# Kernel optimization log

Measured on AMD Instinct MI355X. Metric: run time of the kernel, lower is better.

Reference implementation:

```python
import jax, jax.numpy as jnp
import numpy as np
import math

B, T, IN_DIM = 2, 2048, 512
D, NH, MULT, N_LAYER = 512, 8, 4, 3
N = D * MULT // NH  # per-head latent dim = 256
OUT_DIM = 512
THETA = 2 ** 16


def get_freqs(n):
    t = jnp.arange(n, dtype=jnp.float32)
    q = jnp.floor(t / 2.0) * 2.0  # quantize(q=2)
    return 1.0 / (THETA ** (q / n)) / (2.0 * math.pi)


def ln(x, eps=1e-5):
    mu = jnp.mean(x, axis=-1, keepdims=True)
    var = jnp.var(x, axis=-1, keepdims=True)
    return (x - mu) * jax.lax.rsqrt(var + eps)


def rope(phases, v):
    # phases: [T, N] broadcastable to v [B, nh, T, N]
    p = (phases % 1.0) * (2.0 * math.pi)
    pc, ps = jnp.cos(p), jnp.sin(p)
    # interleave rotate: out[..., 2i] = -v[..., 2i+1], out[..., 2i+1] = v[..., 2i]
    v_rot = jnp.stack((-v[..., 1::2], v[..., ::2]), axis=-1).reshape(v.shape)
    return v * pc + v_rot * ps


def setup_inputs() -> dict:
    key = jax.random.key(0)
    ks = jax.random.split(key, 8)
    std = 0.02
    return {
        "x": jax.random.normal(ks[0], (B, T, IN_DIM), dtype=jnp.float32),
        "w_in": jax.random.normal(ks[1], (IN_DIM, D), dtype=jnp.float32) * std,
        "b_in": jnp.zeros((D,), dtype=jnp.float32),
        "encoder": jax.random.normal(ks[2], (NH, D, N), dtype=jnp.float32) * std,
        "encoder_v": jax.random.normal(ks[3], (NH, D, N), dtype=jnp.float32) * std,
        "decoder": jax.random.normal(ks[4], (NH * N, D), dtype=jnp.float32) * std,
        "head_w": jax.random.normal(ks[5], (D, OUT_DIM), dtype=jnp.float32) * std,
        "head_b": jnp.zeros((OUT_DIM,), dtype=jnp.float32),
    }


def reference(x, w_in, b_in, encoder, encoder_v, decoder, head_w, head_b):
    freqs = get_freqs(N)  # [N]
    t_idx = jnp.arange(T, dtype=jnp.float32)
    phases = t_idx[:, None] * freqs[None, :]  # [T, N]
    # strict lower-triangular causal mask (tril diagonal=-1)
    mask = (jnp.arange(T)[:, None] > jnp.arange(T)[None, :])  # [T, T]
    dec = decoder.reshape(NH, N, D)

    xs = ln(x @ w_in + b_in)  # [B, T, D]
    for _ in range(N_LAYER):
        x_res = xs
        x_sparse = jax.nn.relu(jnp.einsum('btd,hdn->bhtn', xs, encoder))  # [B,nh,T,N]
        QR = rope(phases, x_sparse)
        scores = jnp.einsum('bhtn,bhsn->bhts', QR, QR)
        scores = jnp.where(mask, scores, 0.0)
        yKV = jnp.einsum('bhts,bsd->bhtd', scores, xs)  # V = x (head-broadcast)
        yKV = ln(yKV)
        y_sparse = jax.nn.relu(jnp.einsum('bhtd,hdn->bhtn', yKV, encoder_v))
        xy_sparse = x_sparse * y_sparse  # dropout p=0 -> identity
        yMLP = jnp.einsum('bhtn,hnd->btd', xy_sparse, dec)
        xs = ln(x_res + ln(yMLP))
    logits = xs @ head_w + head_b
    return logits
```

## Files before the change

### kernel.cpp

```cpp
#include <hip/hip_runtime.h>
#include <math.h>

constexpr int B_  = 2;
constexpr int T_  = 2048;
constexpr int D_  = 512;
constexpr int NH_ = 8;
constexpr int NL_ = 256;
constexpr int HN_ = NH_ * NL_;
constexpr int BT_ = B_ * T_;

typedef __bf16 v8bf __attribute__((ext_vector_type(8)));
typedef float  v4f  __attribute__((ext_vector_type(4)));
typedef unsigned short us8 __attribute__((ext_vector_type(8)));
typedef unsigned short us4 __attribute__((ext_vector_type(4)));

__device__ inline unsigned short f2b(float f) {
    union { float f; unsigned u; } v{f};
    unsigned r = v.u + 0x7FFF + ((v.u >> 16) & 1);
    return (unsigned short)(r >> 16);
}
__device__ inline float b2f(unsigned short u) {
    union { unsigned u; float f; } v{(unsigned)u << 16};
    return v.f;
}

__device__ __forceinline__ void g2l16(const void* g, void* l) {
    __builtin_amdgcn_global_load_lds(
        (const __attribute__((address_space(1))) void*)g,
        (__attribute__((address_space(3))) void*)l, 16, 0, 0);
}

#define VMCNT4 asm volatile("s_waitcnt vmcnt(4)" ::: "memory")
#define VMCNT0 asm volatile("s_waitcnt vmcnt(0)" ::: "memory")
#define BARRIER_FENCE                                   \
    __builtin_amdgcn_s_barrier();                       \
    asm volatile("" ::: "memory")

#define TILE_IDS                                              \
    int tid = threadIdx.x;                                    \
    int lane = tid & 63, wid = tid >> 6;                      \
    int wm = (wid & 1) * 64, wn = (wid >> 1) * 64;            \
    int ln16 = lane & 15, q = lane >> 4;                      \
    int srl = lane >> 2, scl = (lane & 3) * 8;                \
    (void)wm; (void)wn;

#define T128_STAGE(Ab, lda, Bb, ldb, k0, buf)                 \
    _Pragma("unroll")                                         \
    for (int ci = 0; ci < 4; ++ci) {                          \
        int c = wid * 4 + ci;                                 \
        if (c < 8) {                                          \
            int r = c * 16 + srl;                             \
            g2l16(Ab + (long)r * lda + (k0) + scl,            \
                  (char*)As[buf] + c * 1024);                 \
        } else {                                              \
            int r = (c - 8) * 16 + srl;                       \
            g2l16(Bb + (long)r * ldb + (k0) + scl,            \
                  (char*)Bs[buf] + (c - 8) * 1024);           \
        }                                                     \
    }

#define TILE_MFMA(Asx, Bsx)                                   \
    {                                                         \
        v8bf af[4], bfr[4];                                   \
        _Pragma("unroll")                                     \
        for (int r = 0; r < 4; ++r)                           \
            af[r] = *(const v8bf*)&Asx[wm + r * 16 + ln16][q * 8]; \
        _Pragma("unroll")                                     \
        for (int c = 0; c < 4; ++c)                           \
            bfr[c] = *(const v8bf*)&Bsx[wn + c * 16 + ln16][q * 8]; \
        _Pragma("unroll")                                     \
        for (int r = 0; r < 4; ++r)                           \
            _Pragma("unroll")                                 \
            for (int c = 0; c < 4; ++c)                       \
                acc[r][c] = __builtin_amdgcn_mfma_f32_16x16x32_bf16( \
                    af[r], bfr[c], acc[r][c], 0, 0, 0);       \
    }

template <int KS, bool RELU, bool MUL, bool BF16OUT, bool LNA>
__global__ __launch_bounds__(256) void gemm128(
    const unsigned short* __restrict__ A, int lda, long sA,
    const unsigned short* __restrict__ Bt, int ldb, long sB,
    void* __restrict__ Cv, int ldc, long sC,
    const unsigned short* __restrict__ mulp, int K,
    const float* __restrict__ muinv, const float* __restrict__ colsum) {
    constexpr int NHF = KS / 32;
    int m0 = blockIdx.y * 128, n0 = blockIdx.x * 128, z = blockIdx.z;
    __shared__ unsigned short As[2][NHF][128][32];
    __shared__ unsigned short Bs[2][NHF][128][32];
    const unsigned short* Ab = A  + (long)z * sA + (long)m0 * lda;
    const unsigned short* Bb = Bt + (long)z * sB + (long)n0 * ldb;
    TILE_IDS
    v4f acc[4][4] = {};
    auto stageK = [&](int k0, int buf) {
        #pragma unroll
        for (int h = 0; h < NHF; ++h)
            #pragma unroll
            for (int ci = 0; ci < 4; ++ci) {
                int c = wid * 4 + ci;
                if (c < 8)
                    g2l16(Ab + (long)(c * 16 + srl) * lda + k0 + h * 32 + scl,
                          (char*)As[buf][h] + c * 1024);
                else
                    g2l16(Bb + (long)((c - 8) * 16 + srl) * ldb + k0 + h * 32 +
                              scl,
                          (char*)Bs[buf][h] + (c - 8) * 1024);
            }
    };
    stageK(0, 0);
    __syncthreads();
    int cur = 0;
    for (int k0 = 0; k0 < K; k0 += KS) {
        if (k0 + KS < K) stageK(k0 + KS, cur ^ 1);
        #pragma unroll
        for (int h = 0; h < NHF; ++h)
            TILE_MFMA(As[cur][h], Bs[cur][h])
        __syncthreads();
        cur ^= 1;
    }
    float* Cf = (float*)Cv;
    unsigned short* Cb = (unsigned short*)Cv;
    long zoff = (long)z * sC;
    #pragma unroll
    for (int r = 0; r < 4; ++r)
        #pragma unroll
        for (int c = 0; c < 4; ++c)
            #pragma unroll
            for (int e = 0; e < 4; ++e) {
                int row = m0 + wm + r * 16 + q * 4 + e;
                int col = n0 + wn + c * 16 + ln16;
                float v = acc[r][c][e];
                if (LNA) {
                    float2 mi = *(const float2*)&muinv[((long)z * BT_ + row) * 2];
                    float cs = colsum[(long)z * NL_ + col];
                    v = mi.y * (v - mi.x * cs);
                }
                if (RELU) v = fmaxf(v, 0.f);
                long idx = zoff + (long)row * ldc + col;
                if (MUL) v *= b2f(mulp[idx]);
                if (BF16OUT) Cb[idx] = f2b(v);
                else         Cf[idx] = v;
            }
}

__global__ __launch_bounds__(256) void enc_rope(
    const unsigned short* __restrict__ A,
    const unsigned short* __restrict__ Bt,
    unsigned short* __restrict__ xsp,
    unsigned short* __restrict__ qrh,
    unsigned short* __restrict__ qrT) {
    int m0 = blockIdx.y * 128, n0 = blockIdx.x * 128;
    __shared__ unsigned short As[4][128][32];
    __shared__ unsigned short Bs[4][128][32];
    unsigned short (*lt)[136] = (unsigned short(*)[136])&As[0][0][0];
    const unsigned short* Ab = A + (long)m0 * 512;
    const unsigned short* Bb = Bt + (long)n0 * 512;
    TILE_IDS
    v4f acc[4][4] = {};
    auto stage = [&](int t) {
        int k0 = t * 32, buf = t & 3;
        #pragma unroll
        for (int ci = 0; ci < 4; ++ci) {
            int c = wid * 4 + ci;
            if (c < 8)
                g2l16(Ab + (long)(c * 16 + srl) * 512 + k0 + scl,
                      (char*)As[buf] + c * 1024);
            else
                g2l16(Bb + (long)((c - 8) * 16 + srl) * 512 + k0 + scl,
                      (char*)Bs[buf] + (c - 8) * 1024);
        }
    };
    stage(0);
    stage(1);
#define ER_STEP(T, W)                                           \
    W;                                                          \
    BARRIER_FENCE;                                              \
    if ((T) + 2 < 16) stage((T) + 2);                           \
    TILE_MFMA(As[(T) & 3], Bs[(T) & 3])
    ER_STEP(0, VMCNT4)  ER_STEP(1, VMCNT4)  ER_STEP(2, VMCNT4)
    ER_STEP(3, VMCNT4)  ER_STEP(4, VMCNT4)  ER_STEP(5, VMCNT4)
    ER_STEP(6, VMCNT4)  ER_STEP(7, VMCNT4)  ER_STEP(8, VMCNT4)
    ER_STEP(9, VMCNT4)  ER_STEP(10, VMCNT4) ER_STEP(11, VMCNT4)
    ER_STEP(12, VMCNT4) ER_STEP(13, VMCNT4) ER_STEP(14, VMCNT4)
    ER_STEP(15, VMCNT0)
#undef ER_STEP
    __syncthreads();
    int bb = m0 >> 11;
    int tbase = m0 & (T_ - 1);
    #pragma unroll
    for (int r = 0; r < 4; ++r)
        #pragma unroll
        for (int c = 0; c < 4; ++c)
            #pragma unroll
            for (int e = 0; e < 4; ++e) {
                int rl = wm + r * 16 + q * 4 + e;
                int col = n0 + wn + c * 16 + ln16;
                float v = fmaxf(acc[r][c][e], 0.f);
                xsp[(long)(m0 + rl) * HN_ + col] = f2b(v);
                int n = col & (NL_ - 1);
                int n2 = n >> 1;
                float fr = exp2f(-(float)n2 * 0.125f) *
                           (float)(1.0 / (2.0 * M_PI));
                float ph = (float)(tbase + rl) * fr;
                ph = (ph - floorf(ph)) * (float)(2.0 * M_PI);
                float s, cc;
                __sincosf(ph, &s, &cc);
                float vp = __shfl_xor(v, 1, 64);
                float o = (n & 1) ? (v * cc + vp * s) : (v * cc - vp * s);
                int hh = col >> 8;
                qrh[((long)(bb * 8 + hh) * T_ + tbase + rl) * NL_ + n] = f2b(o);
                lt[wn + c * 16 + ln16][rl] = f2b(o);
            }
    __syncthreads();
    {
        int nrow = tid >> 1, tseg = (tid & 1) * 64;
        int colg = n0 + nrow;
        int hh = colg >> 8, nn = colg & (NL_ - 1);
        long ob = ((long)(bb * 8 + hh) * NL_ + nn) * T_ + tbase + tseg;
        #pragma unroll
        for (int u = 0; u < 16; ++u)
            *(us4*)&qrT[ob + u * 4] = *(const us4*)&lt[nrow][tseg + u * 4];
    }
}

__global__ __launch_bounds__(256) void ct_gemm(
    const unsigned short* __restrict__ xsT,
    const unsigned short* __restrict__ qrT,
    unsigned short* __restrict__ Ct) {
    int z = blockIdx.x, nt = blockIdx.y;
    int j = blockIdx.z >> 2, mt = blockIdx.z & 3;
    int b = z >> 3;
    const unsigned short* Ab =
        xsT + (long)b * D_ * T_ + (long)(mt * 128) * T_ + j * 256;
    const unsigned short* Bb =
        qrT + (long)z * NL_ * T_ + (long)(nt * 128) * T_ + j * 256;
    __shared__ unsigned short As[2][128][32];
    __shared__ unsigned short Bs[2][128][32];
    TILE_IDS
    v4f acc[4][4] = {};
    T128_STAGE(Ab, T_, Bb, T_, 0, 0)
    __syncthreads();
    int cur = 0;
    for (int k0 = 0; k0 < 256; k0 += 32) {
        if (k0 + 32 < 256) { T128_STAGE(Ab, T_, Bb, T_, k0 + 32, cur ^ 1) }
        TILE_MFMA(As[cur], Bs[cur])
        __syncthreads();
        cur ^= 1;
    }
    unsigned short* ob = Ct + ((long)z * 8 + j) * 512 * 256;
    #pragma unroll
    for (int r = 0; r < 4; ++r)
        #pragma unroll
        for (int c = 0; c < 4; ++c)
            #pragma unroll
            for (int e = 0; e < 4; ++e) {
                int row = mt * 128 + wm + r * 16 + q * 4 + e;
                int col = nt * 128 + wn + c * 16 + ln16;
                ob[(long)row * 256 + col] = f2b(acc[r][c][e]);
            }
}

__global__ __launch_bounds__(256) void prefix_k(unsigned short* __restrict__ Ct) {
    int z = blockIdx.x, dg = blockIdx.y;
    int d = dg * 8 + (threadIdx.x >> 5);
    int n0 = (threadIdx.x & 31) * 8;
    long base = ((long)z * 8) * 512 * 256 + (long)d * 256 + n0;
    constexpr long S = 512 * 256;
    us8 vals[8];
    #pragma unroll
    for (int i = 0; i < 8; ++i)
        vals[i] = *(const us8*)&Ct[base + (long)i * S];
    float acc[8] = {};
    #pragma unroll
    for (int i = 0; i < 8; ++i) {
        us8 o;
        #pragma unroll
        for (int e = 0; e < 8; ++e) o[e] = f2b(acc[e]);
        *(us8*)&Ct[base + (long)i * S] = o;
        #pragma unroll
        for (int e = 0; e < 8; ++e) acc[e] += b2f(vals[i][e]);
    }
}

__global__ __launch_bounds__(256) void sdiag(const unsigned short* __restrict__ qr,
                                             unsigned short* __restrict__ Sd) {
    int z = blockIdx.x, i = blockIdx.y, qq = blockIdx.z;
    int qm = (qq + 1) >> 1, qn = qq >> 1;
    const unsigned short* Ab =
        qr + ((long)z * T_ + i * 256 + qm * 128) * NL_;
    const unsigned short* Bb =
        qr + ((long)z * T_ + i * 256 + qn * 128) * NL_;
    bool dual = (qm != qn);
    __shared__ unsigned short As[2][128][32];
    __shared__ unsigned short Bs[2][128][32];
    TILE_IDS
    v4f acc[4][4] = {};
    auto stg = [&](int k0, int buf) {
        #pragma unroll
        for (int ci = 0; ci < 2; ++ci) {
            int c = wid * 2 + ci;
            g2l16(Ab + (long)(c * 16 + srl) * NL_ + k0 + scl,
                  (char*)As[buf] + c * 1024);
            if (dual)
                g2l16(Bb + (long)(c * 16 + srl) * NL_ + k0 + scl,
                      (char*)Bs[buf] + c * 1024);
        }
    };
    stg(0, 0);
    __syncthreads();
    int cur = 0;
    for (int k0 = 0; k0 < NL_; k0 += 32) {
        if (k0 + 32 < NL_) stg(k0 + 32, cur ^ 1);
        if (dual) { TILE_MFMA(As[cur], Bs[cur]) }
        else      { TILE_MFMA(As[cur], As[cur]) }
        __syncthreads();
        cur ^= 1;
    }
    unsigned short* ob = Sd + ((long)z * 8 + i) * 65536;
    #pragma unroll
    for (int r = 0; r < 4; ++r)
        #pragma unroll
        for (int c = 0; c < 4; ++c)
            #pragma unroll
            for (int e = 0; e < 4; ++e) {
                int row = wm + r * 16 + q * 4 + e;
                int col = wn + c * 16 + ln16;
                float v = acc[r][c][e];
                if (!dual && row <= col) v = 0.f;
                ob[(qm * 128 + row) * 256 + qn * 128 + col] = f2b(v);
            }
}

__global__ __launch_bounds__(256) void pxg(
    const unsigned short* __restrict__ qr,
    const unsigned short* __restrict__ Pt,
    const unsigned short* __restrict__ Sd,
    const unsigned short* __restrict__ xsT,
    unsigned short* __restrict__ ykvu,
    float* __restrict__ part) {
    int z = blockIdx.x, i = blockIdx.y, nt = blockIdx.z;
    int b = z >> 3, h = z & 7;
    int n0 = nt * 128;
    int i256 = i >> 1, hf2 = i & 1;
    const unsigned short* A1 = qr + ((long)z * T_ + i * 128) * NL_;
    const unsigned short* B1 =
        Pt + ((long)z * 8 + i256) * 512 * 256 + (long)n0 * 256;
    const unsigned short* A2 = Sd + ((long)z * 8 + i256) * 65536 +
                               (long)hf2 * 128 * 256;
    const unsigned short* B2 =
        xsT + (long)b * D_ * T_ + (long)n0 * T_ + i256 * 256;
    __shared__ unsigned short As[2][128][32];
    __shared__ unsigned short Bs[2][128][32];
    __shared__ float sred[128][2][2];
    TILE_IDS
    v4f acc[4][4] = {};
    int NS = 12 + hf2 * 4;
    auto stage = [&](int s) {
        const unsigned short* Ap;
        const unsigned short* Bp;
        long lda, ldb;
        int k0;
        if (s < 8) { Ap = A1; lda = NL_; Bp = B1; ldb = 256; k0 = s * 32; }
        else       { Ap = A2; lda = 256; Bp = B2; ldb = T_;  k0 = (s - 8) * 32; }
        int bi = s & 1;
        #pragma unroll
        for (int ci = 0; ci < 4; ++ci) {
            int c = wid * 4 + ci;
            if (c < 8)
                g2l16(Ap + (long)(c * 16 + srl) * lda + k0 + scl,
                      (char*)As[bi] + c * 1024);
            else
                g2l16(Bp + (long)((c - 8) * 16 + srl) * ldb + k0 + scl,
                      (char*)Bs[bi] + (c - 8) * 1024);
        }
    };
    stage(0);
    __syncthreads();
    for (int s = 0; s < NS; ++s) {
        if (s + 1 < NS) stage(s + 1);
        int bi = s & 1;
        TILE_MFMA(As[bi], Bs[bi])
        __syncthreads();
    }
    long obase = ((long)h * BT_ + (long)b * T_ + i * 128) * D_ + n0;
    #pragma unroll
    for (int r = 0; r < 4; ++r) {
        float s1[4] = {}, s2[4] = {};
        #pragma unroll
        for (int c = 0; c < 4; ++c)
            #pragma unroll
            for (int e = 0; e < 4; ++e) {
                float v = acc[r][c][e];
                s1[e] += v;
                s2[e] += v * v;
                int rl = wm + r * 16 + q * 4 + e;
                int col = wn + c * 16 + ln16;
                ykvu[obase + (long)rl * D_ + col] = f2b(v);
            }
        #pragma unroll
        for (int e = 0; e < 4; ++e) {
            #pragma unroll
            for (int off = 1; off < 16; off <<= 1) {
                s1[e] += __shfl_xor(s1[e], off, 64);
                s2[e] += __shfl_xor(s2[e], off, 64);
            }
            if (ln16 == 0) {
                int rl = wm + r * 16 + q * 4 + e;
                sred[rl][wid >> 1][0] = s1[e];
                sred[rl][wid >> 1][1] = s2[e];
            }
        }
    }
    __syncthreads();
    if (tid < 128) {
        float a = sred[tid][0][0] + sred[tid][1][0];
        float sq = sred[tid][0][1] + sred[tid][1][1];
        long pb = ((((long)z * 16 + i) * 4 + nt) * 128 + tid) * 2;
        part[pb] = a;
        part[pb + 1] = sq;
    }
}

__global__ __launch_bounds__(128) void lnstats(const float* __restrict__ part,
                                               float* __restrict__ muinv) {
    int z = blockIdx.x, i = blockIdx.y, t = threadIdx.x;
    long pb = ((((long)z * 16 + i) * 4) * 128 + t) * 2;
    float s1 = part[pb] + part[pb + 256] + part[pb + 512] + part[pb + 768];
    float s2 = part[pb + 1] + part[pb + 257] + part[pb + 513] + part[pb + 769];
    float mu = s1 * (1.0f / 512.0f);
    float var = s2 * (1.0f / 512.0f) - mu * mu;
    float inv = rsqrtf(var + 1e-5f);
    int b = z >> 3, h = z & 7;
    long row = (long)h * BT_ + (long)b * T_ + i * 128 + t;
    muinv[row * 2]     = mu;
    muinv[row * 2 + 1] = inv;
}

__global__ __launch_bounds__(256) void colsum_k(
    const unsigned short* __restrict__ encvT, float* __restrict__ cs) {
    int lane = threadIdx.x & 63, wv = threadIdx.x >> 6;
    int g = blockIdx.x * 4 + wv;
    us8 v = *(const us8*)&encvT[(long)g * 512 + lane * 8];
    float s = 0.f;
    #pragma unroll
    for (int e = 0; e < 8; ++e) s += b2f(v[e]);
    #pragma unroll
    for (int off = 1; off < 64; off <<= 1) s += __shfl_xor(s, off, 64);
    if (lane == 0) cs[g] = s;
}

__global__ __launch_bounds__(256) void trans_cast(
    const float* __restrict__ in, long sIn, unsigned short* __restrict__ out,
    long sOut, int R, int Cc) {
    __shared__ float tl[32][33];
    int z = blockIdx.z;
    int r0 = blockIdx.y * 32, c0 = blockIdx.x * 32;
    int tx = threadIdx.x & 31, ty = threadIdx.x >> 5;
    const float* ip = in + (long)z * sIn;
    unsigned short* op = out + (long)z * sOut;
    #pragma unroll
    for (int j = 0; j < 4; ++j)
        tl[ty + j * 8][tx] = ip[(long)(r0 + ty + j * 8) * Cc + c0 + tx];
    __syncthreads();
    #pragma unroll
    for (int j = 0; j < 4; ++j)
        op[(long)(c0 + ty + j * 8) * R + r0 + tx] = f2b(tl[tx][ty + j * 8]);
}

__global__ __launch_bounds__(256) void trans16(
    const unsigned short* __restrict__ in, long sIn,
    unsigned short* __restrict__ out, long sOut, int R, int Cc) {
    __shared__ unsigned short tl[32][34];
    int z = blockIdx.z;
    int r0 = blockIdx.y * 32, c0 = blockIdx.x * 32;
    int tx = threadIdx.x & 31, ty = threadIdx.x >> 5;
    const unsigned short* ip = in + (long)z * sIn;
    unsigned short* op = out + (long)z * sOut;
    #pragma unroll
    for (int j = 0; j < 4; ++j)
        tl[ty + j * 8][tx] = ip[(long)(r0 + ty + j * 8) * Cc + c0 + tx];
    __syncthreads();
    #pragma unroll
    for (int j = 0; j < 4; ++j)
        op[(long)(c0 + ty + j * 8) * R + r0 + tx] = tl[tx][ty + j * 8];
}

__global__ __launch_bounds__(256) void cast_b(const float* __restrict__ in,
                                              unsigned short* __restrict__ out) {
    long i = ((long)blockIdx.x * 256 + threadIdx.x) * 4;
    float4 v = *(const float4*)&in[i];
    ushort4 o;
    o.x = f2b(v.x); o.y = f2b(v.y); o.z = f2b(v.z); o.w = f2b(v.w);
    *(ushort4*)&out[i] = o;
}

__global__ __launch_bounds__(256) void add_out4(const float* __restrict__ t,
                                                long slice,
                                                const float* __restrict__ bias,
                                                float* __restrict__ o) {
    long i = ((long)blockIdx.x * 256 + threadIdx.x) * 4;
    float4 v0 = *(const float4*)&t[i];
    float4 v1 = *(const float4*)&t[i + slice];
    float4 v2 = *(const float4*)&t[i + 2 * slice];
    float4 v3 = *(const float4*)&t[i + 3 * slice];
    float4 bv = *(const float4*)&bias[i & 511];
    float4 r;
    r.x = v0.x + v1.x + v2.x + v3.x + bv.x;
    r.y = v0.y + v1.y + v2.y + v3.y + bv.y;
    r.z = v0.z + v1.z + v2.z + v3.z + bv.z;
    r.w = v0.w + v1.w + v2.w + v3.w + bv.w;
    *(float4*)&o[i] = r;
}

__device__ inline float2 block_reduce2(float a, float b) {
    __shared__ float sa[4], sb[4];
    #pragma unroll
    for (int off = 32; off; off >>= 1) {
        a += __shfl_down(a, off, 64);
        b += __shfl_down(b, off, 64);
    }
    __syncthreads();
    int w = threadIdx.x >> 6;
    if ((threadIdx.x & 63) == 0) { sa[w] = a; sb[w] = b; }
    __syncthreads();
    return make_float2(sa[0] + sa[1] + sa[2] + sa[3],
                       sb[0] + sb[1] + sb[2] + sb[3]);
}
__device__ inline float2 ln_pair(float2 v) {
    float2 s = block_reduce2(v.x + v.y, 0.f);
    float mu = s.x * (1.0f / 512.0f);
    float dx = v.x - mu, dy = v.y - mu;
    float2 q = block_reduce2(dx * dx + dy * dy, 0.f);
    float inv = rsqrtf(q.x * (1.0f / 512.0f) + 1e-5f);
    return make_float2(dx * inv, dy * inv);
}

__global__ __launch_bounds__(256) void ln_dual4(const float* __restrict__ t,
                                                long slice,
                                                const float* __restrict__ bias,
                                                float* __restrict__ outf,
                                                unsigned short* __restrict__ outb) {
    long row = blockIdx.x;
    int c = threadIdx.x * 2;
    long i = row * 512 + c;
    float2 v0 = *(const float2*)&t[i];
    float2 v1 = *(const float2*)&t[i + slice];
    float2 v2 = *(const float2*)&t[i + 2 * slice];
    float2 v3 = *(const float2*)&t[i + 3 * slice];
    float2 bv = *(const float2*)&bias[c];
    float2 v = make_float2(v0.x + v1.x + v2.x + v3.x + bv.x,
                           v0.y + v1.y + v2.y + v3.y + bv.y);
    float2 o = ln_pair(v);
    *(float2*)&outf[i] = o;
    ushort2 ob; ob.x = f2b(o.x); ob.y = f2b(o.y);
    *(ushort2*)&outb[i] = ob;
}

__global__ __launch_bounds__(256) void combine_dual4(
    const float* __restrict__ t, long slice, const float* __restrict__ xres,
    float* __restrict__ outf, unsigned short* __restrict__ outb) {
    long row = blockIdx.x;
    int c = threadIdx.x * 2;
    long i = row * 512 + c;
    float2 v0 = *(const float2*)&t[i];
    float2 v1 = *(const float2*)&t[i + slice];
    float2 v2 = *(const float2*)&t[i + 2 * slice];
    float2 v3 = *(const float2*)&t[i + 3 * slice];
    float2 y = make_float2(v0.x + v1.x + v2.x + v3.x,
                           v0.y + v1.y + v2.y + v3.y);
    float2 l = ln_pair(y);
    float2 r = *(const float2*)&xres[i];
    float2 z = make_float2(r.x + l.x, r.y + l.y);
    float2 o = ln_pair(z);
    *(float2*)&outf[i] = o;
    ushort2 ob; ob.x = f2b(o.x); ob.y = f2b(o.y);
    *(ushort2*)&outb[i] = ob;
}

extern "C" void kernel_launch(void* const* d_in, const int* in_sizes, int n_in,
                              void* d_out, int out_size, void* d_ws,
                              size_t ws_size, hipStream_t stream) {
    const float* x      = (const float*)d_in[0];
    const float* w_in   = (const float*)d_in[1];
    const float* b_in   = (const float*)d_in[2];
    const float* enc    = (const float*)d_in[3];
    const float* enc_v  = (const float*)d_in[4];
    const float* dec    = (const float*)d_in[5];
    const float* head_w = (const float*)d_in[6];
    const float* head_b = (const float*)d_in[7];
    float* out = (float*)d_out;

    char* w = (char*)d_ws;
    auto alloc = [&](size_t bytes) { void* p = (void*)w; w += bytes; return p; };
    unsigned short* w_inT = (unsigned short*)alloc((size_t)512 * 512 * 2);
    unsigned short* headT = (unsigned short*)alloc((size_t)512 * 512 * 2);
    unsigned short* encT  = (unsigned short*)alloc((size_t)NH_ * NL_ * D_ * 2);
    unsigned short* encvT = (unsigned short*)alloc((size_t)NH_ * NL_ * D_ * 2);
    unsigned short* decT  = (unsigned short*)alloc((size_t)D_ * HN_ * 2);
    unsigned short* xb    = (unsigned short*)alloc((size_t)BT_ * D_ * 2);
    float*          tmp   = (float*)alloc((size_t)4 * BT_ * D_ * 4);
    float*          xsf0  = (float*)alloc((size_t)BT_ * D_ * 4);
    float*          xsf1  = (float*)alloc((size_t)BT_ * D_ * 4);
    unsigned short* xs_b  = (unsigned short*)alloc((size_t)BT_ * D_ * 2);
    unsigned short* xsT   = (unsigned short*)alloc((size_t)B_ * D_ * T_ * 2);
    unsigned short* xsp   = (unsigned short*)alloc((size_t)BT_ * HN_ * 2);
    unsigned short* qrh   = (unsigned short*)alloc((size_t)BT_ * HN_ * 2);
    unsigned short* qrT   = (unsigned short*)alloc((size_t)BT_ * HN_ * 2);
    unsigned short* Ct    = (unsigned short*)alloc((size_t)128 * 512 * 256 * 2);
    unsigned short* Sd    = (unsigned short*)alloc((size_t)128 * 256 * 256 * 2);
    unsigned short* ykv   = (unsigned short*)alloc((size_t)NH_ * BT_ * D_ * 2);
    float*          part  = (float*)alloc((size_t)256 * 4 * 128 * 2 * 4);
    float*          muinv = (float*)alloc((size_t)NH_ * BT_ * 2 * 4);
    float*          csum  = (float*)alloc((size_t)HN_ * 4);
    const long SL = (long)BT_ * D_;

    cast_b<<<BT_ * D_ / 1024, 256, 0, stream>>>(x, xb);
    trans_cast<<<dim3(16, 16, 1), 256, 0, stream>>>(w_in, 0, w_inT, 0, 512, 512);
    trans_cast<<<dim3(16, 16, 1), 256, 0, stream>>>(head_w, 0, headT, 0, 512, 512);
    trans_cast<<<dim3(8, 16, 8), 256, 0, stream>>>(enc, (long)D_ * NL_, encT,
                                                   (long)NL_ * D_, D_, NL_);
    trans_cast<<<dim3(8, 16, 8), 256, 0, stream>>>(enc_v, (long)D_ * NL_, encvT,
                                                   (long)NL_ * D_, D_, NL_);
    trans_cast<<<dim3(16, 64, 1), 256, 0, stream>>>(dec, 0, decT, 0, HN_, D_);
    colsum_k<<<HN_ / 4, 256, 0, stream>>>(encvT, csum);

    gemm128<64, false, false, false, false>
        <<<dim3(4, 32, 4), 256, 0, stream>>>(xb, D_, 128, w_inT, D_, 128, tmp,
                                             D_, SL, nullptr, 128, nullptr,
                                             nullptr);
    ln_dual4<<<BT_, 256, 0, stream>>>(tmp, SL, b_in, xsf0, xs_b);
    trans16<<<dim3(16, 64, 2), 256, 0, stream>>>(xs_b, (long)T_ * D_, xsT,
                                                 (long)D_ * T_, T_, D_);

    float* xin = xsf0;
    float* xout = xsf1;
    for (int l = 0; l < 3; ++l) {
        enc_rope<<<dim3(16, 32), 256, 0, stream>>>(xs_b, encT, xsp, qrh, qrT);
        ct_gemm<<<dim3(16, 2, 32), 256, 0, stream>>>(xsT, qrT, Ct);
        prefix_k<<<dim3(16, 64), 256, 0, stream>>>(Ct);
        sdiag<<<dim3(16, 8, 3), 256, 0, stream>>>(qrh, Sd);
        pxg<<<dim3(16, 16, 4), 256, 0, stream>>>(qrh, Ct, Sd, xsT, ykv, part);
        lnstats<<<dim3(16, 16), 128, 0, stream>>>(part, muinv);
        gemm128<64, true, true, true, true>
            <<<dim3(2, 32, 8), 256, 0, stream>>>(
                ykv, D_, (long)BT_ * D_, encvT, D_, (long)NL_ * D_, xsp, HN_,
                NL_, xsp, 512, muinv, csum);
        gemm128<64, false, false, false, false>
            <<<dim3(4, 32, 4), 256, 0, stream>>>(
                xsp, HN_, 512, decT, HN_, 512, tmp, D_, SL, nullptr, 512,
                nullptr, nullptr);
        combine_dual4<<<BT_, 256, 0, stream>>>(tmp, SL, xin, xout, xs_b);
        trans16<<<dim3(16, 64, 2), 256, 0, stream>>>(xs_b, (long)T_ * D_, xsT,
                                                     (long)D_ * T_, T_, D_);
        float* t = xin; xin = xout; xout = t;
    }

    gemm128<64, false, false, false, false>
        <<<dim3(4, 32, 4), 256, 0, stream>>>(xs_b, D_, 128, headT, D_, 128, tmp,
                                             D_, SL, nullptr, 128, nullptr,
                                             nullptr);
    add_out4<<<BT_ * 512 / 1024, 256, 0, stream>>>(tmp, SL, head_b, out);
}
```

Before: 597.5 us.

## Merge independent kernels into combined launches and fold LN stats into GEMM

Puts the xs transpose into the same launch as the encoder+RoPE GEMM, dispatching on block index. The Ct GEMM and the diagonal score kernel are combined the same way. The separate lnstats kernel is removed: the LN-A GEMM now reduces the partial sums into shared memory before its main loop. This cuts launches and lets independent work fill the GPU at the same time. In exchange, the transpose blocks reserve the full 64KB shared allocation sized for the GEMM blocks, and the stats reduction is repeated in every column tile.

```diff
diff --git a/kernel.cpp b/kernel.cpp
--- a/kernel.cpp
+++ b/kernel.cpp
@@ -43,21 +43,6 @@
     int ln16 = lane & 15, q = lane >> 4;                      \
     int srl = lane >> 2, scl = (lane & 3) * 8;                \
     (void)wm; (void)wn;
-
-#define T128_STAGE(Ab, lda, Bb, ldb, k0, buf)                 \
-    _Pragma("unroll")                                         \
-    for (int ci = 0; ci < 4; ++ci) {                          \
-        int c = wid * 4 + ci;                                 \
-        if (c < 8) {                                          \
-            int r = c * 16 + srl;                             \
-            g2l16(Ab + (long)r * lda + (k0) + scl,            \
-                  (char*)As[buf] + c * 1024);                 \
-        } else {                                              \
-            int r = (c - 8) * 16 + srl;                       \
-            g2l16(Bb + (long)r * ldb + (k0) + scl,            \
-                  (char*)Bs[buf] + (c - 8) * 1024);           \
-        }                                                     \
-    }
 
 #define TILE_MFMA(Asx, Bsx)                                   \
     {                                                         \
@@ -82,11 +67,12 @@
     const unsigned short* __restrict__ Bt, int ldb, long sB,
     void* __restrict__ Cv, int ldc, long sC,
     const unsigned short* __restrict__ mulp, int K,
-    const float* __restrict__ muinv, const float* __restrict__ colsum) {
+    const float* __restrict__ part, const float* __restrict__ colsum) {
     constexpr int NHF = KS / 32;
     int m0 = blockIdx.y * 128, n0 = blockIdx.x * 128, z = blockIdx.z;
     __shared__ unsigned short As[2][NHF][128][32];
     __shared__ unsigned short Bs[2][NHF][128][32];
+    __shared__ float muis[128][2];
     const unsigned short* Ab = A  + (long)z * sA + (long)m0 * lda;
     const unsigned short* Bb = Bt + (long)z * sB + (long)n0 * ldb;
     TILE_IDS
@@ -107,6 +93,19 @@
             }
     };
     stageK(0, 0);
+    if (LNA && tid < 128) {
+        int bb = m0 >> 11;
+        int ii = (m0 & (T_ - 1)) >> 7;
+        int zp = bb * 8 + z;
+        long pb = ((((long)zp * 16 + ii) * 4) * 128 + tid) * 2;
+        float s1 = part[pb] + part[pb + 256] + part[pb + 512] + part[pb + 768];
+        float s2 =
+            part[pb + 1] + part[pb + 257] + part[pb + 513] + part[pb + 769];
+        float mu = s1 * (1.0f / 512.0f);
+        float var = s2 * (1.0f / 512.0f) - mu * mu;
+        muis[tid][0] = mu;
+        muis[tid][1] = rsqrtf(var + 1e-5f);
+    }
     __syncthreads();
     int cur = 0;
     for (int k0 = 0; k0 < K; k0 += KS) {
@@ -126,13 +125,13 @@
         for (int c = 0; c < 4; ++c)
             #pragma unroll
             for (int e = 0; e < 4; ++e) {
-                int row = m0 + wm + r * 16 + q * 4 + e;
+                int lrow = wm + r * 16 + q * 4 + e;
+                int row = m0 + lrow;
                 int col = n0 + wn + c * 16 + ln16;
                 float v = acc[r][c][e];
                 if (LNA) {
-                    float2 mi = *(const float2*)&muinv[((long)z * BT_ + row) * 2];
                     float cs = colsum[(long)z * NL_ + col];
-                    v = mi.y * (v - mi.x * cs);
+                    v = muis[lrow][1] * (v - muis[lrow][0] * cs);
                 }
                 if (RELU) v = fmaxf(v, 0.f);
                 long idx = zoff + (long)row * ldc + col;
@@ -142,16 +141,17 @@
             }
 }
 
-__global__ __launch_bounds__(256) void enc_rope(
+__device__ __forceinline__ void enc_body(
     const unsigned short* __restrict__ A,
     const unsigned short* __restrict__ Bt,
     unsigned short* __restrict__ xsp,
     unsigned short* __restrict__ qrh,
-    unsigned short* __restrict__ qrT) {
-    int m0 = blockIdx.y * 128, n0 = blockIdx.x * 128;
-    __shared__ unsigned short As[4][128][32];
-    __shared__ unsigned short Bs[4][128][32];
-    unsigned short (*lt)[136] = (unsigned short(*)[136])&As[0][0][0];
+    unsigned short* __restrict__ qrT,
+    unsigned short* smem, int nt, int mt) {
+    int m0 = mt * 128, n0 = nt * 128;
+    auto As = (unsigned short(*)[128][32])smem;
+    auto Bs = (unsigned short(*)[128][32])(smem + 16384);
+    unsigned short (*lt)[136] = (unsigned short(*)[136])smem;
     const unsigned short* Ab = A + (long)m0 * 512;
     const unsigned short* Bb = Bt + (long)n0 * 512;
     TILE_IDS
@@ -222,26 +222,67 @@
     }
 }
 
-__global__ __launch_bounds__(256) void ct_gemm(
-    const unsigned short* __restrict__ xsT,
-    const unsigned short* __restrict__ qrT,
-    unsigned short* __restrict__ Ct) {
-    int z = blockIdx.x, nt = blockIdx.y;
-    int j = blockIdx.z >> 2, mt = blockIdx.z & 3;
+__device__ __forceinline__ void tr_body(const unsigned short* __restrict__ in,
+                                        unsigned short* __restrict__ out,
+                                        unsigned short* smem, int tb) {
+    unsigned short (*tl)[34] = (unsigned short(*)[34])smem;
+    int x = tb & 15, y = (tb >> 4) & 63, zz = tb >> 10;
+    int r0 = y * 32, c0 = x * 32;
+    int tx = threadIdx.x & 31, ty = threadIdx.x >> 5;
+    const unsigned short* ip = in + (long)zz * T_ * D_;
+    unsigned short* op = out + (long)zz * D_ * T_;
+    #pragma unroll
+    for (int j = 0; j < 4; ++j)
+        tl[ty + j * 8][tx] = ip[(long)(r0 + ty + j * 8) * D_ + c0 + tx];
+    __syncthreads();
+    #pragma unroll
+    for (int j = 0; j < 4; ++j)
+        op[(long)(c0 + ty + j * 8) * T_ + r0 + tx] = tl[tx][ty + j * 8];
+}
+
+__global__ __launch_bounds__(256) void enc_tr(
+    const unsigned short* __restrict__ A, const unsigned short* __restrict__ Bt,
+    unsigned short* __restrict__ xsp, unsigned short* __restrict__ qrh,
+    unsigned short* __restrict__ qrT, unsigned short* __restrict__ xsT) {
+    __shared__ unsigned short smem[32768];
+    int bid = blockIdx.x;
+    if (bid < 512)
+        enc_body(A, Bt, xsp, qrh, qrT, smem, bid & 15, bid >> 4);
+    else
+        tr_body(A, xsT, smem, bid - 512);
+}
+
+__device__ __forceinline__ void ct_body(
+    const unsigned short* __restrict__ xsT, const unsigned short* __restrict__ qrT,
+    unsigned short* __restrict__ Ct, unsigned short* smem,
+    int z, int nt, int jm) {
+    int j = jm >> 2, mt = jm & 3;
     int b = z >> 3;
+    auto As = (unsigned short(*)[128][32])smem;
+    auto Bs = (unsigned short(*)[128][32])(smem + 8192);
     const unsigned short* Ab =
         xsT + (long)b * D_ * T_ + (long)(mt * 128) * T_ + j * 256;
     const unsigned short* Bb =
         qrT + (long)z * NL_ * T_ + (long)(nt * 128) * T_ + j * 256;
-    __shared__ unsigned short As[2][128][32];
-    __shared__ unsigned short Bs[2][128][32];
     TILE_IDS
     v4f acc[4][4] = {};
-    T128_STAGE(Ab, T_, Bb, T_, 0, 0)
+    auto stg = [&](int k0, int buf) {
+        #pragma unroll
+        for (int ci = 0; ci < 4; ++ci) {
+            int c = wid * 4 + ci;
+            if (c < 8)
+                g2l16(Ab + (long)(c * 16 + srl) * T_ + k0 + scl,
+                      (char*)As[buf] + c * 1024);
+            else
+                g2l16(Bb + (long)((c - 8) * 16 + srl) * T_ + k0 + scl,
+                      (char*)Bs[buf] + (c - 8) * 1024);
+        }
+    };
+    stg(0, 0);
     __syncthreads();
     int cur = 0;
     for (int k0 = 0; k0 < 256; k0 += 32) {
-        if (k0 + 32 < 256) { T128_STAGE(Ab, T_, Bb, T_, k0 + 32, cur ^ 1) }
+        if (k0 + 32 < 256) stg(k0 + 32, cur ^ 1);
         TILE_MFMA(As[cur], Bs[cur])
         __syncthreads();
         cur ^= 1;
@@ -259,39 +300,18 @@
             }
 }
 
-__global__ __launch_bounds__(256) void prefix_k(unsigned short* __restrict__ Ct) {
-    int z = blockIdx.x, dg = blockIdx.y;
-    int d = dg * 8 + (threadIdx.x >> 5);
-    int n0 = (threadIdx.x & 31) * 8;
-    long base = ((long)z * 8) * 512 * 256 + (long)d * 256 + n0;
-    constexpr long S = 512 * 256;
-    us8 vals[8];
-    #pragma unroll
-    for (int i = 0; i < 8; ++i)
-        vals[i] = *(const us8*)&Ct[base + (long)i * S];
-    float acc[8] = {};
-    #pragma unroll
-    for (int i = 0; i < 8; ++i) {
-        us8 o;
-        #pragma unroll
-        for (int e = 0; e < 8; ++e) o[e] = f2b(acc[e]);
-        *(us8*)&Ct[base + (long)i * S] = o;
-        #pragma unroll
-        for (int e = 0; e < 8; ++e) acc[e] += b2f(vals[i][e]);
-    }
-}
-
-__global__ __launch_bounds__(256) void sdiag(const unsigned short* __restrict__ qr,
-                                             unsigned short* __restrict__ Sd) {
-    int z = blockIdx.x, i = blockIdx.y, qq = blockIdx.z;
+__device__ __forceinline__ void sd_body(const unsigned short* __restrict__ qr,
+                                        unsigned short* __restrict__ Sd,
+                                        unsigned short* smem,
+                                        int z, int i, int qq) {
     int qm = (qq + 1) >> 1, qn = qq >> 1;
+    auto As = (unsigned short(*)[128][32])smem;
+    auto Bs = (unsigned short(*)[128][32])(smem + 8192);
     const unsigned short* Ab =
         qr + ((long)z * T_ + i * 256 + qm * 128) * NL_;
     const unsigned short* Bb =
         qr + ((long)z * T_ + i * 256 + qn * 128) * NL_;
     bool dual = (qm != qn);
-    __shared__ unsigned short As[2][128][32];
-    __shared__ unsigned short Bs[2][128][32];
     TILE_IDS
     v4f acc[4][4] = {};
     auto stg = [&](int k0, int buf) {
@@ -328,6 +348,43 @@
                 if (!dual && row <= col) v = 0.f;
                 ob[(qm * 128 + row) * 256 + qn * 128 + col] = f2b(v);
             }
+}
+
+__global__ __launch_bounds__(256) void ct_sd(
+    const unsigned short* __restrict__ xsT,
+    const unsigned short* __restrict__ qrT,
+    const unsigned short* __restrict__ qrh,
+    unsigned short* __restrict__ Ct, unsigned short* __restrict__ Sd) {
+    __shared__ unsigned short smem[16384];
+    int bid = blockIdx.x;
+    if (bid < 1024)
+        ct_body(xsT, qrT, Ct, smem, bid & 15, (bid >> 4) & 1, bid >> 5);
+    else {
+        int sid = bid - 1024;
+        sd_body(qrh, Sd, smem, sid & 15, (sid >> 4) & 7, sid >> 7);
+    }
+}
+
+__global__ __launch_bounds__(256) void prefix_k(unsigned short* __restrict__ Ct) {
+    int z = blockIdx.x, dg = blockIdx.y;
+    int d = dg * 8 + (threadIdx.x >> 5);
+    int n0 = (threadIdx.x & 31) * 8;
+    long base = ((long)z * 8) * 512 * 256 + (long)d * 256 + n0;
+    constexpr long S = 512 * 256;
+    us8 vals[8];
+    #pragma unroll
+    for (int i = 0; i < 8; ++i)
+        vals[i] = *(const us8*)&Ct[base + (long)i * S];
+    float acc[8] = {};
+    #pragma unroll
+    for (int i = 0; i < 8; ++i) {
+        us8 o;
+        #pragma unroll
+        for (int e = 0; e < 8; ++e) o[e] = f2b(acc[e]);
+        *(us8*)&Ct[base + (long)i * S] = o;
+        #pragma unroll
+        for (int e = 0; e < 8; ++e) acc[e] += b2f(vals[i][e]);
+    }
 }
 
 __global__ __launch_bounds__(256) void pxg(
@@ -420,21 +477,6 @@
     }
 }
 
-__global__ __launch_bounds__(128) void lnstats(const float* __restrict__ part,
-                                               float* __restrict__ muinv) {
-    int z = blockIdx.x, i = blockIdx.y, t = threadIdx.x;
-    long pb = ((((long)z * 16 + i) * 4) * 128 + t) * 2;
-    float s1 = part[pb] + part[pb + 256] + part[pb + 512] + part[pb + 768];
-    float s2 = part[pb + 1] + part[pb + 257] + part[pb + 513] + part[pb + 769];
-    float mu = s1 * (1.0f / 512.0f);
-    float var = s2 * (1.0f / 512.0f) - mu * mu;
-    float inv = rsqrtf(var + 1e-5f);
-    int b = z >> 3, h = z & 7;
-    long row = (long)h * BT_ + (long)b * T_ + i * 128 + t;
-    muinv[row * 2]     = mu;
-    muinv[row * 2 + 1] = inv;
-}
-
 __global__ __launch_bounds__(256) void colsum_k(
     const unsigned short* __restrict__ encvT, float* __restrict__ cs) {
     int lane = threadIdx.x & 63, wv = threadIdx.x >> 6;
@@ -464,24 +506,6 @@
     #pragma unroll
     for (int j = 0; j < 4; ++j)
         op[(long)(c0 + ty + j * 8) * R + r0 + tx] = f2b(tl[tx][ty + j * 8]);
-}
-
-__global__ __launch_bounds__(256) void trans16(
-    const unsigned short* __restrict__ in, long sIn,
-    unsigned short* __restrict__ out, long sOut, int R, int Cc) {
-    __shared__ unsigned short tl[32][34];
-    int z = blockIdx.z;
-    int r0 = blockIdx.y * 32, c0 = blockIdx.x * 32;
-    int tx = threadIdx.x & 31, ty = threadIdx.x >> 5;
-    const unsigned short* ip = in + (long)z * sIn;
-    unsigned short* op = out + (long)z * sOut;
-    #pragma unroll
-    for (int j = 0; j < 4; ++j)
-        tl[ty + j * 8][tx] = ip[(long)(r0 + ty + j * 8) * Cc + c0 + tx];
-    __syncthreads();
-    #pragma unroll
-    for (int j = 0; j < 4; ++j)
-        op[(long)(c0 + ty + j * 8) * R + r0 + tx] = tl[tx][ty + j * 8];
 }
 
 __global__ __launch_bounds__(256) void cast_b(const float* __restrict__ in,
@@ -609,7 +633,6 @@
     unsigned short* Sd    = (unsigned short*)alloc((size_t)128 * 256 * 256 * 2);
     unsigned short* ykv   = (unsigned short*)alloc((size_t)NH_ * BT_ * D_ * 2);
     float*          part  = (float*)alloc((size_t)256 * 4 * 128 * 2 * 4);
-    float*          muinv = (float*)alloc((size_t)NH_ * BT_ * 2 * 4);
     float*          csum  = (float*)alloc((size_t)HN_ * 4);
     const long SL = (long)BT_ * D_;
 
@@ -628,29 +651,23 @@
                                              D_, SL, nullptr, 128, nullptr,
                                              nullptr);
     ln_dual4<<<BT_, 256, 0, stream>>>(tmp, SL, b_in, xsf0, xs_b);
-    trans16<<<dim3(16, 64, 2), 256, 0, stream>>>(xs_b, (long)T_ * D_, xsT,
-                                                 (long)D_ * T_, T_, D_);
 
     float* xin = xsf0;
     float* xout = xsf1;
     for (int l = 0; l < 3; ++l) {
-        enc_rope<<<dim3(16, 32), 256, 0, stream>>>(xs_b, encT, xsp, qrh, qrT);
-        ct_gemm<<<dim3(16, 2, 32), 256, 0, stream>>>(xsT, qrT, Ct);
+        enc_tr<<<2560, 256, 0, stream>>>(xs_b, encT, xsp, qrh, qrT, xsT);
+        ct_sd<<<1408, 256, 0, stream>>>(xsT, qrT, qrh, Ct, Sd);
         prefix_k<<<dim3(16, 64), 256, 0, stream>>>(Ct);
-        sdiag<<<dim3(16, 8, 3), 256, 0, stream>>>(qrh, Sd);
         pxg<<<dim3(16, 16, 4), 256, 0, stream>>>(qrh, Ct, Sd, xsT, ykv, part);
-        lnstats<<<dim3(16, 16), 128, 0, stream>>>(part, muinv);
         gemm128<64, true, true, true, true>
             <<<dim3(2, 32, 8), 256, 0, stream>>>(
                 ykv, D_, (long)BT_ * D_, encvT, D_, (long)NL_ * D_, xsp, HN_,
-                NL_, xsp, 512, muinv, csum);
+                NL_, xsp, 512, part, csum);
         gemm128<64, false, false, false, false>
             <<<dim3(4, 32, 4), 256, 0, stream>>>(
                 xsp, HN_, 512, decT, HN_, 512, tmp, D_, SL, nullptr, 512,
                 nullptr, nullptr);
         combine_dual4<<<BT_, 256, 0, stream>>>(tmp, SL, xin, xout, xs_b);
-        trans16<<<dim3(16, 64, 2), 256, 0, stream>>>(xs_b, (long)T_ * D_, xsT,
-                                                     (long)D_ * T_, T_, D_);
         float* t = xin; xin = xout; xout = t;
     }
 
```

Result: faster. 550.1 us (-7.9%).
